# Optimization experiments

Hardware: AMD Instinct MI355X
Metric: run time of the kernel (lower is better)

Reference implementation:

```python
import jax, jax.numpy as jnp
import numpy as np

B, LQ, LK, H, A = 32, 2048, 2048, 1024, 512


def setup_inputs() -> dict:
    key = jax.random.key(0)
    ks = jax.random.split(key, 5)
    s = 1.0 / np.sqrt(H)
    return {
        "query": jax.random.normal(ks[0], (B, LQ, H), jnp.float32),
        "key": jax.random.normal(ks[1], (B, LK, H), jnp.float32),
        "Wq": jax.random.normal(ks[2], (H, A), jnp.float32) * s,
        "bq": jnp.zeros((A,), jnp.float32),
        "Wk": jax.random.normal(ks[3], (H, A), jnp.float32) * s,
        "bk": jnp.zeros((A,), jnp.float32),
        "Wv": jax.random.normal(ks[4], (A, 1), jnp.float32) * (1.0 / np.sqrt(A)),
        "bv": jnp.zeros((1,), jnp.float32),
    }


def reference(query, key, Wq, bq, Wk, bk, Wv, bv):
    # Linear projections
    Qp = jnp.einsum("bqh,ha->bqa", query, Wq) + bq          # [B, LQ, A]
    Kp = jnp.einsum("bkh,ha->bka", key, Wk) + bk            # [B, LK, A]
    # Score matrix Q(query) @ K(key)^T
    alpha_mat = jnp.einsum("bqa,bka->bqk", Qp, Kp)          # [B, LQ, LK]
    # Sum over query dim, softmax over key dim
    alpha = jax.nn.softmax(alpha_mat.sum(axis=1, keepdims=True), axis=2)  # [B, 1, LK]
    # Per-key scalar head V applied to projected keys, then weighted combine
    v = jnp.einsum("bka,ao->bko", Kp, Wv) + bv              # [B, LK, 1]
    x = jnp.matmul(alpha, v)[:, 0, :]                        # [B, 1]
    return x
```

## Files before the change

kernel.cpp:

```cpp
#include <hip/hip_runtime.h>
#include <math.h>

#define NB 32
#define LQ 2048
#define LK 2048
#define HD 1024
#define AD 512
#define QCH 32

__global__ void __launch_bounds__(256) k1_qreduce(const float* __restrict__ query,
                                                 float* __restrict__ partial) {
    int bid = blockIdx.x;
    int b = bid / QCH, qc = bid % QCH;
    int t = threadIdx.x;
    const int QPC = LQ / QCH;
    float4 a0 = {0.f, 0.f, 0.f, 0.f};
    float4 a1 = {0.f, 0.f, 0.f, 0.f};
    const float4* src = (const float4*)(query + ((size_t)b * LQ + (size_t)qc * QPC) * HD);
    for (int q = 0; q < QPC; q += 2) {
        float4 v0 = src[(size_t)q * (HD / 4) + t];
        float4 v1 = src[(size_t)(q + 1) * (HD / 4) + t];
        a0.x += v0.x; a0.y += v0.y; a0.z += v0.z; a0.w += v0.w;
        a1.x += v1.x; a1.y += v1.y; a1.z += v1.z; a1.w += v1.w;
    }
    float4 acc = {a0.x + a1.x, a0.y + a1.y, a0.z + a1.z, a0.w + a1.w};
    float4* dst = (float4*)(partial + ((size_t)qc * NB + b) * HD);
    dst[t] = acc;
}

__global__ void __launch_bounds__(256) k2_qreduce2(const float* __restrict__ partial,
                                                   float* __restrict__ s_q) {
    int t = blockIdx.x * blockDim.x + threadIdx.x;
    float acc = 0.f;
    for (int qc = 0; qc < QCH; ++qc) acc += partial[(size_t)qc * NB * HD + t];
    s_q[t] = acc;
}

__global__ void __launch_bounds__(256) k3_qsum(const float* __restrict__ s_q,
                                               const float* __restrict__ Wq,
                                               const float* __restrict__ bq,
                                               float* __restrict__ qsum) {
    int t = blockIdx.x * blockDim.x + threadIdx.x;
    int b = t / AD, a = t % AD;
    const float* sr = s_q + (size_t)b * HD;
    const float* wp = Wq + a;
    double c0 = 0.0, c1 = 0.0, c2 = 0.0, c3 = 0.0;
    for (int h = 0; h < HD; h += 4) {
        c0 += (double)sr[h]     * (double)wp[(size_t)h * AD];
        c1 += (double)sr[h + 1] * (double)wp[(size_t)(h + 1) * AD];
        c2 += (double)sr[h + 2] * (double)wp[(size_t)(h + 2) * AD];
        c3 += (double)sr[h + 3] * (double)wp[(size_t)(h + 3) * AD];
    }
    qsum[t] = (float)(((c0 + c1) + (c2 + c3)) + (double)LQ * (double)bq[a]);
}

__global__ void __launch_bounds__(256) k4_weff(const float* __restrict__ qsum,
                                               const float* __restrict__ Wk,
                                               const float* __restrict__ Wv,
                                               const float* __restrict__ bk,
                                               const float* __restrict__ bv,
                                               float* __restrict__ wk_eff,
                                               float* __restrict__ wv_eff,
                                               float* __restrict__ c_v) {
    int w = threadIdx.x >> 6, lane = threadIdx.x & 63;
    int widx = blockIdx.x * 4 + w;
    double acc = 0.0;
    if (widx < NB * HD) {
        int b = widx / HD, h = widx % HD;
        const float4* wr = (const float4*)(Wk + (size_t)h * AD);
        const float4* qs = (const float4*)(qsum + (size_t)b * AD);
        #pragma unroll
        for (int j = 0; j < 2; ++j) {
            int f = lane + 64 * j;
            float4 wv4 = wr[f];
            float4 q4  = qs[f];
            acc += (double)wv4.x * (double)q4.x + (double)wv4.y * (double)q4.y
                 + (double)wv4.z * (double)q4.z + (double)wv4.w * (double)q4.w;
        }
        #pragma unroll
        for (int off = 32; off > 0; off >>= 1) acc += __shfl_down(acc, off);
        if (lane == 0) wk_eff[widx] = (float)acc;
    } else if (widx < NB * HD + HD) {
        int h = widx - NB * HD;
        const float4* wr = (const float4*)(Wk + (size_t)h * AD);
        const float4* vv = (const float4*)(Wv);
        #pragma unroll
        for (int j = 0; j < 2; ++j) {
            int f = lane + 64 * j;
            float4 wv4 = wr[f];
            float4 v4  = vv[f];
            acc += (double)wv4.x * (double)v4.x + (double)wv4.y * (double)v4.y
                 + (double)wv4.z * (double)v4.z + (double)wv4.w * (double)v4.w;
        }
        #pragma unroll
        for (int off = 32; off > 0; off >>= 1) acc += __shfl_down(acc, off);
        if (lane == 0) wv_eff[h] = (float)acc;
    } else if (widx == NB * HD + HD) {
        const float4* br = (const float4*)(bk);
        const float4* vv = (const float4*)(Wv);
        #pragma unroll
        for (int j = 0; j < 2; ++j) {
            int f = lane + 64 * j;
            float4 b4 = br[f];
            float4 v4 = vv[f];
            acc += (double)b4.x * (double)v4.x + (double)b4.y * (double)v4.y
                 + (double)b4.z * (double)v4.z + (double)b4.w * (double)v4.w;
        }
        #pragma unroll
        for (int off = 32; off > 0; off >>= 1) acc += __shfl_down(acc, off);
        if (lane == 0) c_v[0] = (float)(acc + (double)bv[0]);
    }
}

__global__ void __launch_bounds__(256) k5_scores(const float* __restrict__ key,
                                                 const float* __restrict__ wk_eff,
                                                 const float* __restrict__ wv_eff,
                                                 const float* __restrict__ c_v,
                                                 float* __restrict__ scores,
                                                 float* __restrict__ vvals) {
    __shared__ float lwk[HD];
    __shared__ float lwv[HD];
    int bid = blockIdx.x;
    int b = bid >> 6;
    int k0 = (bid & 63) * 32;
    for (int i = threadIdx.x; i < HD; i += 256) {
        lwk[i] = wk_eff[(size_t)b * HD + i];
        lwv[i] = wv_eff[i];
    }
    __syncthreads();
    int w = threadIdx.x >> 6;
    int lane = threadIdx.x & 63;
    double cv = (double)c_v[0];
    const float4* lwk4 = (const float4*)lwk;
    const float4* lwv4 = (const float4*)lwv;
    for (int r = 0; r < 8; ++r) {
        int k = k0 + w * 8 + r;
        const float4* kr = (const float4*)(key + ((size_t)b * LK + k) * HD);
        double sc = 0.0, vv = 0.0;
        #pragma unroll
        for (int j = 0; j < 4; ++j) {
            int f = lane + 64 * j;
            float4 kv  = kr[f];
            float4 wk4 = lwk4[f];
            float4 wv4 = lwv4[f];
            sc += (double)kv.x * (double)wk4.x + (double)kv.y * (double)wk4.y
                + (double)kv.z * (double)wk4.z + (double)kv.w * (double)wk4.w;
            vv += (double)kv.x * (double)wv4.x + (double)kv.y * (double)wv4.y
                + (double)kv.z * (double)wv4.z + (double)kv.w * (double)wv4.w;
        }
        #pragma unroll
        for (int off = 32; off > 0; off >>= 1) {
            sc += __shfl_down(sc, off);
            vv += __shfl_down(vv, off);
        }
        if (lane == 0) {
            scores[(size_t)b * LK + k] = (float)sc;
            vvals[(size_t)b * LK + k]  = (float)(vv + cv);
        }
    }
}

__global__ void __launch_bounds__(256) k6_softmax(const float* __restrict__ scores,
                                                  const float* __restrict__ vvals,
                                                  float* __restrict__ out) {
    int b = blockIdx.x;
    int t = threadIdx.x;
    __shared__ float smax_sh[4];
    __shared__ double num_sh[4], den_sh[4];
    const float* sr = scores + (size_t)b * LK;
    const float* vr = vvals  + (size_t)b * LK;
    float m = -INFINITY;
    for (int k = t; k < LK; k += 256) m = fmaxf(m, sr[k]);
    #pragma unroll
    for (int off = 32; off > 0; off >>= 1) m = fmaxf(m, __shfl_down(m, off));
    int w = t >> 6, lane = t & 63;
    if (lane == 0) smax_sh[w] = m;
    __syncthreads();
    float gm = fmaxf(fmaxf(smax_sh[0], smax_sh[1]), fmaxf(smax_sh[2], smax_sh[3]));
    double num = 0.0, den = 0.0;
    for (int k = t; k < LK; k += 256) {
        double e = exp((double)(sr[k] - gm));
        den += e;
        num += e * (double)vr[k];
    }
    #pragma unroll
    for (int off = 32; off > 0; off >>= 1) {
        num += __shfl_down(num, off);
        den += __shfl_down(den, off);
    }
    if (lane == 0) { num_sh[w] = num; den_sh[w] = den; }
    __syncthreads();
    if (t == 0) {
        double N = num_sh[0] + num_sh[1] + num_sh[2] + num_sh[3];
        double D = den_sh[0] + den_sh[1] + den_sh[2] + den_sh[3];
        out[b] = (float)(N / D);
    }
}

extern "C" void kernel_launch(void* const* d_in, const int* in_sizes, int n_in,
                              void* d_out, int out_size, void* d_ws, size_t ws_size,
                              hipStream_t stream) {
    const float* query = (const float*)d_in[0];
    const float* key   = (const float*)d_in[1];
    const float* Wq    = (const float*)d_in[2];
    const float* bq    = (const float*)d_in[3];
    const float* Wk    = (const float*)d_in[4];
    const float* bk    = (const float*)d_in[5];
    const float* Wv    = (const float*)d_in[6];
    const float* bv    = (const float*)d_in[7];
    float* out = (float*)d_out;

    float* ws = (float*)d_ws;
    size_t off = 0;
    float* partial = ws + off; off += (size_t)QCH * NB * HD;
    float* s_q     = ws + off; off += (size_t)NB * HD;
    float* qsum    = ws + off; off += (size_t)NB * AD;
    float* wk_eff  = ws + off; off += (size_t)NB * HD;
    float* wv_eff  = ws + off; off += (size_t)HD;
    float* c_v     = ws + off; off += 1;
    float* scores  = ws + off; off += (size_t)NB * LK;
    float* vvals   = ws + off; off += (size_t)NB * LK;

    hipLaunchKernelGGL(k1_qreduce, dim3(NB * QCH), dim3(256), 0, stream, query, partial);
    hipLaunchKernelGGL(k2_qreduce2, dim3(NB * HD / 256), dim3(256), 0, stream, partial, s_q);
    hipLaunchKernelGGL(k3_qsum, dim3(NB * AD / 256), dim3(256), 0, stream, s_q, Wq, bq, qsum);
    hipLaunchKernelGGL(k4_weff, dim3((NB * HD + HD + 1 + 3) / 4), dim3(256), 0, stream,
                       qsum, Wk, Wv, bk, bv, wk_eff, wv_eff, c_v);
    hipLaunchKernelGGL(k5_scores, dim3(NB * (LK / 32)), dim3(256), 0, stream,
                       key, wk_eff, wv_eff, c_v, scores, vvals);
    hipLaunchKernelGGL(k6_softmax, dim3(NB), dim3(256), 0, stream, scores, vvals, out);
}
```

Baseline: 163.1 us.

## Fuse query partial reduction into qsum kernel and move Wv terms into first kernel

The second-stage reduction of query partials is merged into the Wq projection kernel, which now reduces into shared memory and splits the H dimension across four waves with a shared-memory combine. The Wk·Wv and bk·Wv dot products move out of k4 into extra blocks of the first kernel so they run alongside the query reduction. This drops one launch and the s_q round trip through global memory, and raises parallelism in the serial qsum matvec. In exchange each qsum block re-reads the partials for its batch, eight times per batch.

```diff
diff --git a/kernel.cpp b/kernel.cpp
--- a/kernel.cpp
+++ b/kernel.cpp
@@ -9,107 +9,132 @@
 #define QCH 32
 
 __global__ void __launch_bounds__(256) k1_qreduce(const float* __restrict__ query,
-                                                 float* __restrict__ partial) {
+                                                 const float* __restrict__ Wk,
+                                                 const float* __restrict__ Wv,
+                                                 const float* __restrict__ bk,
+                                                 const float* __restrict__ bv,
+                                                 float* __restrict__ partial,
+                                                 float* __restrict__ wv_eff,
+                                                 float* __restrict__ c_v) {
     int bid = blockIdx.x;
-    int b = bid / QCH, qc = bid % QCH;
-    int t = threadIdx.x;
-    const int QPC = LQ / QCH;
-    float4 a0 = {0.f, 0.f, 0.f, 0.f};
-    float4 a1 = {0.f, 0.f, 0.f, 0.f};
-    const float4* src = (const float4*)(query + ((size_t)b * LQ + (size_t)qc * QPC) * HD);
-    for (int q = 0; q < QPC; q += 2) {
-        float4 v0 = src[(size_t)q * (HD / 4) + t];
-        float4 v1 = src[(size_t)(q + 1) * (HD / 4) + t];
-        a0.x += v0.x; a0.y += v0.y; a0.z += v0.z; a0.w += v0.w;
-        a1.x += v1.x; a1.y += v1.y; a1.z += v1.z; a1.w += v1.w;
-    }
-    float4 acc = {a0.x + a1.x, a0.y + a1.y, a0.z + a1.z, a0.w + a1.w};
-    float4* dst = (float4*)(partial + ((size_t)qc * NB + b) * HD);
-    dst[t] = acc;
-}
-
-__global__ void __launch_bounds__(256) k2_qreduce2(const float* __restrict__ partial,
-                                                   float* __restrict__ s_q) {
-    int t = blockIdx.x * blockDim.x + threadIdx.x;
-    float acc = 0.f;
-    for (int qc = 0; qc < QCH; ++qc) acc += partial[(size_t)qc * NB * HD + t];
-    s_q[t] = acc;
-}
-
-__global__ void __launch_bounds__(256) k3_qsum(const float* __restrict__ s_q,
+    if (bid < NB * QCH) {
+        int b = bid / QCH, qc = bid % QCH;
+        int t = threadIdx.x;
+        const int QPC = LQ / QCH;
+        float4 a0 = {0.f, 0.f, 0.f, 0.f};
+        float4 a1 = {0.f, 0.f, 0.f, 0.f};
+        const float4* src = (const float4*)(query + ((size_t)b * LQ + (size_t)qc * QPC) * HD);
+        for (int q = 0; q < QPC; q += 2) {
+            float4 v0 = src[(size_t)q * (HD / 4) + t];
+            float4 v1 = src[(size_t)(q + 1) * (HD / 4) + t];
+            a0.x += v0.x; a0.y += v0.y; a0.z += v0.z; a0.w += v0.w;
+            a1.x += v1.x; a1.y += v1.y; a1.z += v1.z; a1.w += v1.w;
+        }
+        float4 acc = {a0.x + a1.x, a0.y + a1.y, a0.z + a1.z, a0.w + a1.w};
+        float4* dst = (float4*)(partial + ((size_t)qc * NB + b) * HD);
+        dst[t] = acc;
+    } else if (bid < NB * QCH + 16) {
+        int w = threadIdx.x >> 6, lane = threadIdx.x & 63;
+        int gw = (bid - NB * QCH) * 4 + w;
+        const float4* vv = (const float4*)(Wv);
+        for (int r = 0; r < 16; ++r) {
+            int h = gw * 16 + r;
+            const float4* wr = (const float4*)(Wk + (size_t)h * AD);
+            double acc = 0.0;
+            #pragma unroll
+            for (int j = 0; j < 2; ++j) {
+                int f = lane + 64 * j;
+                float4 w4 = wr[f];
+                float4 v4 = vv[f];
+                acc += (double)w4.x * (double)v4.x + (double)w4.y * (double)v4.y
+                     + (double)w4.z * (double)v4.z + (double)w4.w * (double)v4.w;
+            }
+            #pragma unroll
+            for (int off = 32; off > 0; off >>= 1) acc += __shfl_down(acc, off);
+            if (lane == 0) wv_eff[h] = (float)acc;
+        }
+    } else {
+        if (threadIdx.x < 64) {
+            int lane = threadIdx.x;
+            const float4* br = (const float4*)(bk);
+            const float4* vv = (const float4*)(Wv);
+            double acc = 0.0;
+            #pragma unroll
+            for (int j = 0; j < 2; ++j) {
+                int f = lane + 64 * j;
+                float4 b4 = br[f];
+                float4 v4 = vv[f];
+                acc += (double)b4.x * (double)v4.x + (double)b4.y * (double)v4.y
+                     + (double)b4.z * (double)v4.z + (double)b4.w * (double)v4.w;
+            }
+            #pragma unroll
+            for (int off = 32; off > 0; off >>= 1) acc += __shfl_down(acc, off);
+            if (lane == 0) c_v[0] = (float)(acc + (double)bv[0]);
+        }
+    }
+}
+
+__global__ void __launch_bounds__(256) kB_qsum(const float* __restrict__ partial,
                                                const float* __restrict__ Wq,
                                                const float* __restrict__ bq,
                                                float* __restrict__ qsum) {
-    int t = blockIdx.x * blockDim.x + threadIdx.x;
-    int b = t / AD, a = t % AD;
-    const float* sr = s_q + (size_t)b * HD;
+    __shared__ float sq[HD];
+    __shared__ double red[4][64];
+    int b = blockIdx.x >> 3;
+    int a0 = (blockIdx.x & 7) * 64;
+    int t = threadIdx.x;
+
+    #pragma unroll
+    for (int c = 0; c < 4; ++c) {
+        int h = t + c * 256;
+        float acc = 0.f;
+        #pragma unroll 4
+        for (int qc = 0; qc < QCH; ++qc)
+            acc += partial[((size_t)qc * NB + b) * HD + h];
+        sq[h] = acc;
+    }
+    __syncthreads();
+
+    int w = t >> 6, lane = t & 63;
+    int a = a0 + lane;
     const float* wp = Wq + a;
     double c0 = 0.0, c1 = 0.0, c2 = 0.0, c3 = 0.0;
-    for (int h = 0; h < HD; h += 4) {
-        c0 += (double)sr[h]     * (double)wp[(size_t)h * AD];
-        c1 += (double)sr[h + 1] * (double)wp[(size_t)(h + 1) * AD];
-        c2 += (double)sr[h + 2] * (double)wp[(size_t)(h + 2) * AD];
-        c3 += (double)sr[h + 3] * (double)wp[(size_t)(h + 3) * AD];
-    }
-    qsum[t] = (float)(((c0 + c1) + (c2 + c3)) + (double)LQ * (double)bq[a]);
+    int hbase = w * 256;
+    for (int i = 0; i < 256; i += 4) {
+        int h = hbase + i;
+        c0 += (double)sq[h]     * (double)wp[(size_t)h * AD];
+        c1 += (double)sq[h + 1] * (double)wp[(size_t)(h + 1) * AD];
+        c2 += (double)sq[h + 2] * (double)wp[(size_t)(h + 2) * AD];
+        c3 += (double)sq[h + 3] * (double)wp[(size_t)(h + 3) * AD];
+    }
+    red[w][lane] = ((c0 + c1) + (c2 + c3));
+    __syncthreads();
+    if (t < 64) {
+        double s = red[0][t] + red[1][t] + red[2][t] + red[3][t];
+        qsum[(size_t)b * AD + a0 + t] = (float)(s + (double)LQ * (double)bq[a0 + t]);
+    }
 }
 
 __global__ void __launch_bounds__(256) k4_weff(const float* __restrict__ qsum,
                                                const float* __restrict__ Wk,
-                                               const float* __restrict__ Wv,
-                                               const float* __restrict__ bk,
-                                               const float* __restrict__ bv,
-                                               float* __restrict__ wk_eff,
-                                               float* __restrict__ wv_eff,
-                                               float* __restrict__ c_v) {
+                                               float* __restrict__ wk_eff) {
     int w = threadIdx.x >> 6, lane = threadIdx.x & 63;
     int widx = blockIdx.x * 4 + w;
+    int b = widx >> 10, h = widx & (HD - 1);
+    const float4* wr = (const float4*)(Wk + (size_t)h * AD);
+    const float4* qs = (const float4*)(qsum + (size_t)b * AD);
     double acc = 0.0;
-    if (widx < NB * HD) {
-        int b = widx / HD, h = widx % HD;
-        const float4* wr = (const float4*)(Wk + (size_t)h * AD);
-        const float4* qs = (const float4*)(qsum + (size_t)b * AD);
-        #pragma unroll
-        for (int j = 0; j < 2; ++j) {
-            int f = lane + 64 * j;
-            float4 wv4 = wr[f];
-            float4 q4  = qs[f];
-            acc += (double)wv4.x * (double)q4.x + (double)wv4.y * (double)q4.y
-                 + (double)wv4.z * (double)q4.z + (double)wv4.w * (double)q4.w;
-        }
-        #pragma unroll
-        for (int off = 32; off > 0; off >>= 1) acc += __shfl_down(acc, off);
-        if (lane == 0) wk_eff[widx] = (float)acc;
-    } else if (widx < NB * HD + HD) {
-        int h = widx - NB * HD;
-        const float4* wr = (const float4*)(Wk + (size_t)h * AD);
-        const float4* vv = (const float4*)(Wv);
-        #pragma unroll
-        for (int j = 0; j < 2; ++j) {
-            int f = lane + 64 * j;
-            float4 wv4 = wr[f];
-            float4 v4  = vv[f];
-            acc += (double)wv4.x * (double)v4.x + (double)wv4.y * (double)v4.y
-                 + (double)wv4.z * (double)v4.z + (double)wv4.w * (double)v4.w;
-        }
-        #pragma unroll
-        for (int off = 32; off > 0; off >>= 1) acc += __shfl_down(acc, off);
-        if (lane == 0) wv_eff[h] = (float)acc;
-    } else if (widx == NB * HD + HD) {
-        const float4* br = (const float4*)(bk);
-        const float4* vv = (const float4*)(Wv);
-        #pragma unroll
-        for (int j = 0; j < 2; ++j) {
-            int f = lane + 64 * j;
-            float4 b4 = br[f];
-            float4 v4 = vv[f];
-            acc += (double)b4.x * (double)v4.x + (double)b4.y * (double)v4.y
-                 + (double)b4.z * (double)v4.z + (double)b4.w * (double)v4.w;
-        }
-        #pragma unroll
-        for (int off = 32; off > 0; off >>= 1) acc += __shfl_down(acc, off);
-        if (lane == 0) c_v[0] = (float)(acc + (double)bv[0]);
-    }
+    #pragma unroll
+    for (int j = 0; j < 2; ++j) {
+        int f = lane + 64 * j;
+        float4 w4 = wr[f];
+        float4 q4 = qs[f];
+        acc += (double)w4.x * (double)q4.x + (double)w4.y * (double)q4.y
+             + (double)w4.z * (double)q4.z + (double)w4.w * (double)q4.w;
+    }
+    #pragma unroll
+    for (int off = 32; off > 0; off >>= 1) acc += __shfl_down(acc, off);
+    if (lane == 0) wk_eff[widx] = (float)acc;
 }
 
 __global__ void __launch_bounds__(256) k5_scores(const float* __restrict__ key,
@@ -213,7 +238,6 @@
     float* ws = (float*)d_ws;
     size_t off = 0;
     float* partial = ws + off; off += (size_t)QCH * NB * HD;
-    float* s_q     = ws + off; off += (size_t)NB * HD;
     float* qsum    = ws + off; off += (size_t)NB * AD;
     float* wk_eff  = ws + off; off += (size_t)NB * HD;
     float* wv_eff  = ws + off; off += (size_t)HD;
@@ -221,11 +245,10 @@
     float* scores  = ws + off; off += (size_t)NB * LK;
     float* vvals   = ws + off; off += (size_t)NB * LK;
 
-    hipLaunchKernelGGL(k1_qreduce, dim3(NB * QCH), dim3(256), 0, stream, query, partial);
-    hipLaunchKernelGGL(k2_qreduce2, dim3(NB * HD / 256), dim3(256), 0, stream, partial, s_q);
-    hipLaunchKernelGGL(k3_qsum, dim3(NB * AD / 256), dim3(256), 0, stream, s_q, Wq, bq, qsum);
-    hipLaunchKernelGGL(k4_weff, dim3((NB * HD + HD + 1 + 3) / 4), dim3(256), 0, stream,
-                       qsum, Wk, Wv, bk, bv, wk_eff, wv_eff, c_v);
+    hipLaunchKernelGGL(k1_qreduce, dim3(NB * QCH + 16 + 1), dim3(256), 0, stream,
+                       query, Wk, Wv, bk, bv, partial, wv_eff, c_v);
+    hipLaunchKernelGGL(kB_qsum, dim3(NB * 8), dim3(256), 0, stream, partial, Wq, bq, qsum);
+    hipLaunchKernelGGL(k4_weff, dim3(NB * HD / 4), dim3(256), 0, stream, qsum, Wk, wk_eff);
     hipLaunchKernelGGL(k5_scores, dim3(NB * (LK / 32)), dim3(256), 0, stream,
                        key, wk_eff, wv_eff, c_v, scores, vvals);
     hipLaunchKernelGGL(k6_softmax, dim3(NB), dim3(256), 0, stream, scores, vvals, out);
```

Result: faster. 148.6 us (-8.9%).
